# Optimization experiments

Measured on AMD Instinct MI355X. Metric: run time of the kernel, lower is better.

## Reference

```python
import jax, jax.numpy as jnp
import numpy as np

N = 100000   # nodes
E = 1600000  # edges
R = 8        # num_relations = 2 * n_speakers**2, n_speakers=2
G = 128      # g_dim
H1 = 64      # h1_dim
H2 = 64      # h2_dim (heads=1, concat)
NEG_SLOPE_ATT = 0.2   # RGATConv default negative_slope
NEG_SLOPE_OUT = 0.01  # F.leaky_relu default
BN_EPS = 1e-5


def setup_inputs() -> dict:
    key = jax.random.key(0)
    ks = jax.random.split(key, 13)
    node_features = jax.random.normal(ks[0], (N, G), dtype=jnp.float32)
    edge_index = jax.random.randint(ks[1], (2, E), 0, N, dtype=jnp.int64)
    edge_type = jax.random.randint(ks[2], (E,), 0, R, dtype=jnp.int64)
    # RGATConv layer 1: per-relation weight [R, in, heads*out], q/k [heads*out, heads], bias
    W1 = jax.random.normal(ks[3], (R, G, H1), dtype=jnp.float32) / np.float32(np.sqrt(G))
    q1 = jax.random.normal(ks[4], (H1, 1), dtype=jnp.float32) / np.float32(np.sqrt(H1))
    k1 = jax.random.normal(ks[5], (H1, 1), dtype=jnp.float32) / np.float32(np.sqrt(H1))
    b1 = jnp.zeros((H1,), dtype=jnp.float32)
    # RGATConv layer 2
    W2 = jax.random.normal(ks[6], (R, H1, H2), dtype=jnp.float32) / np.float32(np.sqrt(H1))
    q2 = jax.random.normal(ks[7], (H2, 1), dtype=jnp.float32) / np.float32(np.sqrt(H2))
    k2 = jax.random.normal(ks[8], (H2, 1), dtype=jnp.float32) / np.float32(np.sqrt(H2))
    b2 = jnp.zeros((H2,), dtype=jnp.float32)
    # BatchNorm1d affine params
    gamma = jnp.ones((H2,), dtype=jnp.float32)
    beta = jnp.zeros((H2,), dtype=jnp.float32)
    return {"node_features": node_features, "edge_index": edge_index,
            "edge_type": edge_type, "W1": W1, "q1": q1, "k1": k1, "b1": b1,
            "W2": W2, "q2": q2, "k2": k2, "b2": b2, "gamma": gamma, "beta": beta}


def _rgat_conv(x, src, dst, edge_type, W, q, k, b):
    # Per-relation dense transform for all nodes: [R, N, O] (R is small = 8)
    xw = jnp.einsum('ni,rio->rno', x, W)
    # Per-edge transformed endpoint features (gathered by relation + node id)
    hi = xw[edge_type, dst]   # [E, O] target-side
    hj = xw[edge_type, src]   # [E, O] source-side (message content)
    # Additive self-attention, across-relation softmax over incoming edges of dst
    alpha = jax.nn.leaky_relu(hi @ q + hj @ k, NEG_SLOPE_ATT)  # [E, 1]
    n = x.shape[0]
    m = jax.ops.segment_max(alpha, dst, num_segments=n)
    m = jnp.where(jnp.isfinite(m), m, 0.0)  # nodes with no in-edges
    e = jnp.exp(alpha - m[dst])
    denom = jax.ops.segment_sum(e, dst, num_segments=n)
    a = e / (denom[dst] + 1e-16)
    # Weighted scatter-add aggregation (heads=1, concat)
    out = jax.ops.segment_sum(hj * a, dst, num_segments=n)  # [N, O]
    return out + b


def reference(node_features, edge_index, edge_type, W1, q1, k1, b1,
              W2, q2, k2, b2, gamma, beta):
    src = edge_index[0]  # source j (messages flow src -> dst)
    dst = edge_index[1]  # target i
    x = _rgat_conv(node_features, src, dst, edge_type, W1, q1, k1, b1)
    x = jax.nn.relu(x)
    x = _rgat_conv(x, src, dst, edge_type, W2, q2, k2, b2)
    # BatchNorm1d (training-mode batch statistics, biased variance)
    mean = jnp.mean(x, axis=0)
    var = jnp.var(x, axis=0)
    x = (x - mean) * jax.lax.rsqrt(var + BN_EPS) * gamma + beta
    return jax.nn.leaky_relu(x, NEG_SLOPE_OUT)
```

## Files before the change

kernel.cpp:

```cpp
#include <hip/hip_runtime.h>
#include <hip/hip_bf16.h>

#define NN 100000
#define EE 1600000
#define RR 8
#define NBKT 391
#define ACHUNK 2048
#define CAP 5120
#define NB_NODES ((NN + 63) / 64)

typedef __attribute__((ext_vector_type(8))) short bf16x8;
typedef __attribute__((ext_vector_type(4))) float f32x4;

__device__ __forceinline__ unsigned short f2bf(float v) {
    __hip_bfloat16 h = __float2bfloat16(v);
    return *reinterpret_cast<unsigned short*>(&h);
}
__device__ __forceinline__ float bf2f(unsigned short u) {
    unsigned x = (unsigned)u << 16;
    return __uint_as_float(x);
}

template<int IN_DIM>
__device__ __forceinline__ void wt_frag_dev(const float* __restrict__ W,
                                            unsigned short* __restrict__ Wf,
                                            int r, int blk, int nb) {
    constexpr int KSTEPS = IN_DIM / 32;
    for (int i = blk * 256 + threadIdx.x; i < IN_DIM * 64; i += nb * 256) {
        int k = i >> 6, o = i & 63;
        int ks = k >> 5, quad = (k >> 3) & 3, j = k & 7;
        int tl = o >> 4, l16 = o & 15;
        int lane = quad * 16 + l16;
        size_t idx = ((((size_t)r * KSTEPS + ks) * 4 + tl) * 64 + lane) * 8 + j;
        Wf[idx] = f2bf(W[((size_t)r * IN_DIM + k) * 64 + o]);
    }
}

template<int IN_DIM>
__device__ __forceinline__ void wqk_frag_dev(const float* __restrict__ W,
        const float* __restrict__ q, const float* __restrict__ k,
        unsigned short* __restrict__ Sf, int blk, int nb) {
    for (int i = blk * 256 + threadIdx.x; i < IN_DIM * 16; i += nb * 256) {
        int j = i & 7, lane = (i >> 3) & 63, ks = i >> 9;
        int col = lane & 15, quad = lane >> 4;
        int kd = ks * 32 + quad * 8 + j;
        const float* v = (col < 8) ? q : k;
        int r = (col < 8) ? col : col - 8;
        float s = 0.f;
        #pragma unroll
        for (int o = 0; o < 64; o++) s += W[((size_t)r * IN_DIM + kd) * 64 + o] * v[o];
        Sf[i] = f2bf(s);
    }
}

__global__ __launch_bounds__(256)
void prep(const float* __restrict__ W1, const float* __restrict__ q1, const float* __restrict__ k1,
          const float* __restrict__ W2, const float* __restrict__ q2, const float* __restrict__ k2,
          unsigned short* __restrict__ Wf1, unsigned short* __restrict__ Wf2,
          unsigned short* __restrict__ Sf1, unsigned short* __restrict__ Sf2,
          unsigned* __restrict__ bcnt, float* __restrict__ stats)
{
    int b = blockIdx.x;
    if (b < 16)       wt_frag_dev<128>(W1, Wf1, b >> 1, b & 1, 2);
    else if (b < 32)  wt_frag_dev<64>(W2, Wf2, (b - 16) >> 1, b & 1, 2);
    else if (b < 48)  wqk_frag_dev<128>(W1, q1, k1, Sf1, b - 32, 16);
    else if (b < 52)  wqk_frag_dev<64>(W2, q2, k2, Sf2, b - 48, 4);
    else {
        int t = threadIdx.x;
        for (int i = t; i < NBKT; i += 256) bcnt[i] = 0;
        if (t < 128) stats[t] = 0.f;
    }
}

__global__ __launch_bounds__(256)
void part_scatter(const int* __restrict__ src, const int* __restrict__ dst,
                  const int* __restrict__ et, unsigned* __restrict__ bcnt,
                  unsigned* __restrict__ tmp) {
    __shared__ unsigned h[NBKT], base[NBKT];
    int t = threadIdx.x;
    for (int i = t; i < NBKT; i += 256) h[i] = 0;
    __syncthreads();
    int e0 = blockIdx.x * ACHUNK;
    for (int i = t; i < ACHUNK; i += 256) {
        int e = e0 + i;
        if (e < EE) atomicAdd(&h[((unsigned)dst[e]) >> 8], 1u);
    }
    __syncthreads();
    for (int i = t; i < NBKT; i += 256) {
        base[i] = (unsigned)i * CAP + (h[i] ? atomicAdd(&bcnt[i], h[i]) : 0u);
        h[i] = 0;
    }
    __syncthreads();
    for (int i = t; i < ACHUNK; i += 256) {
        int e = e0 + i;
        if (e < EE) {
            unsigned d = (unsigned)dst[e];
            unsigned bk = d >> 8;
            unsigned off = atomicAdd(&h[bk], 1u);
            unsigned pos = base[bk] + off;
            if (pos < (bk + 1u) * CAP) {
                unsigned val = ((d & 255u) << 23) | ((unsigned)et[e] << 20) | (unsigned)src[e];
                tmp[pos] = val;
            }
        }
    }
}

__global__ __launch_bounds__(256)
void bucket_csr(const unsigned* __restrict__ bcnt, const unsigned* __restrict__ tmp,
                unsigned* __restrict__ rowstart, unsigned* __restrict__ rowdeg,
                unsigned* __restrict__ pk) {
    __shared__ unsigned lcnt[256], lscan[256], lrs[256];
    int b = blockIdx.x, t = threadIdx.x;
    unsigned ebeg = (unsigned)b * CAP;
    unsigned cnt = min(bcnt[b], (unsigned)CAP);
    unsigned eend = ebeg + cnt;
    lcnt[t] = 0;
    __syncthreads();
    for (unsigned i = ebeg + t; i < eend; i += 256)
        atomicAdd(&lcnt[tmp[i] >> 23], 1u);
    __syncthreads();
    unsigned v = lcnt[t];
    lscan[t] = v;
    __syncthreads();
    for (int off = 1; off < 256; off <<= 1) {
        unsigned u = (t >= off) ? lscan[t - off] : 0u;
        __syncthreads();
        lscan[t] += u;
        __syncthreads();
    }
    unsigned excl = lscan[t] - v;
    lrs[t] = ebeg + excl;
    int node = b * 256 + t;
    if (node < NN) { rowstart[node] = ebeg + excl; rowdeg[node] = v; }
    lcnt[t] = 0;
    __syncthreads();
    for (unsigned i = ebeg + t; i < eend; i += 256) {
        unsigned val = tmp[i];
        unsigned d = val >> 23;
        unsigned pos = lrs[d] + atomicAdd(&lcnt[d], 1u);
        pk[pos] = val & 0x7FFFFFu;
    }
}

template<int IN_DIM, bool BF16IN>
__global__ __launch_bounds__(256)
void gemm_mfma(const void* __restrict__ xv, const unsigned short* __restrict__ Wf,
               const unsigned short* __restrict__ Sf,
               unsigned short* __restrict__ xw,
               float* __restrict__ sq, float* __restrict__ sk,
               float* __restrict__ gmax)
{
    constexpr int KSTEPS = IN_DIM / 32;
    constexpr int NB = IN_DIM / 8;
    constexpr int WITEMS = KSTEPS * 4 * 64;
    __shared__ alignas(16) unsigned short xl[64 * IN_DIM];
    __shared__ alignas(16) unsigned short wl[WITEMS * 8];
    __shared__ float smax[4][8];

    const int n0 = blockIdx.x * 64;
    const int t = threadIdx.x;
    const int wave = t >> 6, lane = t & 63;
    const int quad = lane >> 4, l16 = lane & 15;

    for (int c = t; c < 64 * IN_DIM / 4; c += 256) {
        int row = c / (IN_DIM / 4), kc = (c % (IN_DIM / 4)) * 4;
        int gr = n0 + row;
        ushort4 u = make_ushort4(0, 0, 0, 0);
        if constexpr (BF16IN) {
            if (gr < NN) u = *(const ushort4*)((const unsigned short*)xv + (size_t)gr * IN_DIM + kc);
        } else {
            if (gr < NN) {
                float4 v = *(const float4*)((const float*)xv + (size_t)gr * IN_DIM + kc);
                u.x = f2bf(v.x); u.y = f2bf(v.y); u.z = f2bf(v.z); u.w = f2bf(v.w);
            }
        }
        int b = kc >> 3;
        *(ushort4*)&xl[row * IN_DIM + ((b ^ (row & (NB - 1))) << 3) + (kc & 7)] = u;
    }
    __syncthreads();

    bf16x8 afr[KSTEPS];
    const int arow = wave * 16 + l16;
    #pragma unroll
    for (int ks = 0; ks < KSTEPS; ks++) {
        int b = ks * 4 + quad;
        afr[ks] = *(const bf16x8*)&xl[arow * IN_DIM + ((b ^ (arow & (NB - 1))) << 3)];
    }

    {
        f32x4 accs = {0.f, 0.f, 0.f, 0.f};
        #pragma unroll
        for (int ks = 0; ks < KSTEPS; ks++) {
            bf16x8 sfr = *(const bf16x8*)&Sf[(ks * 64 + lane) * 8];
            accs = __builtin_amdgcn_mfma_f32_16x16x32_bf16(afr[ks], sfr, accs, 0, 0, 0);
        }
        float pm = -1e30f;
        #pragma unroll
        for (int reg = 0; reg < 4; reg++) {
            int grow = n0 + wave * 16 + quad * 4 + reg;
            if (grow < NN) {
                if (l16 < 8) sq[(size_t)l16 * NN + grow] = accs[reg];
                else { sk[(size_t)(l16 - 8) * NN + grow] = accs[reg]; pm = fmaxf(pm, accs[reg]); }
            }
        }
        pm = fmaxf(pm, __shfl_xor(pm, 16, 64));
        pm = fmaxf(pm, __shfl_xor(pm, 32, 64));
        if (quad == 0 && l16 >= 8) smax[wave][l16 - 8] = pm;
    }
    __syncthreads();
    if (t < 8) {
        float v = fmaxf(fmaxf(smax[0][t], smax[1][t]), fmaxf(smax[2][t], smax[3][t]));
        gmax[blockIdx.x * 8 + t] = v;
    }

    #pragma unroll 1
    for (int r = 0; r < RR; r++) {
        const unsigned short* Wr = Wf + (size_t)r * WITEMS * 8;
        #pragma unroll
        for (int i = t; i < WITEMS; i += 256)
            *(bf16x8*)&wl[(size_t)i * 8] = *(const bf16x8*)(Wr + (size_t)i * 8);
        __syncthreads();

        bf16x8 bfr[KSTEPS][4];
        #pragma unroll
        for (int ks = 0; ks < KSTEPS; ks++)
            #pragma unroll
            for (int tl = 0; tl < 4; tl++)
                bfr[ks][tl] = *(const bf16x8*)&wl[(size_t)((ks * 4 + tl) * 64 + lane) * 8];

        f32x4 acc[4] = {{0.f,0.f,0.f,0.f},{0.f,0.f,0.f,0.f},{0.f,0.f,0.f,0.f},{0.f,0.f,0.f,0.f}};
        #pragma unroll
        for (int ks = 0; ks < KSTEPS; ks++)
            #pragma unroll
            for (int tl = 0; tl < 4; tl++)
                acc[tl] = __builtin_amdgcn_mfma_f32_16x16x32_bf16(afr[ks], bfr[ks][tl], acc[tl], 0, 0, 0);

        const size_t rbase = (size_t)r * NN;
        #pragma unroll
        for (int reg = 0; reg < 4; reg++) {
            int grow = n0 + wave * 16 + quad * 4 + reg;
            if (grow < NN) {
                ushort4 u;
                u.x = f2bf(acc[0][reg]); u.y = f2bf(acc[1][reg]);
                u.z = f2bf(acc[2][reg]); u.w = f2bf(acc[3][reg]);
                *(ushort4*)(xw + (rbase + grow) * 64 + l16 * 4) = u;
            }
        }
        __syncthreads();
    }
}

__global__ __launch_bounds__(256)
void max_reduce(const float* __restrict__ gmax, float* __restrict__ mxk) {
    __shared__ float smr[32][8];
    int t = threadIdx.x;
    int r = t & 7, grp = t >> 3;
    float m0 = -1e30f, m1 = -1e30f, m2 = -1e30f, m3 = -1e30f;
    for (int i = grp; i < NB_NODES; i += 128) {
        m0 = fmaxf(m0, gmax[i * 8 + r]);
        int i1 = i + 32, i2 = i + 64, i3 = i + 96;
        if (i1 < NB_NODES) m1 = fmaxf(m1, gmax[i1 * 8 + r]);
        if (i2 < NB_NODES) m2 = fmaxf(m2, gmax[i2 * 8 + r]);
        if (i3 < NB_NODES) m3 = fmaxf(m3, gmax[i3 * 8 + r]);
    }
    smr[grp][r] = fmaxf(fmaxf(m0, m1), fmaxf(m2, m3));
    __syncthreads();
    if (t < 8) {
        float mm = smr[0][t];
        #pragma unroll
        for (int g2 = 1; g2 < 32; g2++) mm = fmaxf(mm, smr[g2][t]);
        mxk[t] = mm;
    }
}

template<int LAYER>
__global__ __launch_bounds__(256)
void node_aggregate(const unsigned* __restrict__ rowstart, const unsigned* __restrict__ rowdeg,
                    const unsigned* __restrict__ pk,
                    const float* __restrict__ sq, const float* __restrict__ sk,
                    const float* __restrict__ mxk,
                    const unsigned short* __restrict__ xw, const float* __restrict__ b,
                    void* __restrict__ outv)
{
    const int node = blockIdx.x * 4 + (threadIdx.x >> 6);
    const int lane = threadIdx.x & 63;
    const int g = lane >> 4, c16 = lane & 15;
    const unsigned beg = rowstart[node];
    const unsigned deg = rowdeg[node];
    const unsigned end = beg + deg;

    const float sqreg = sq[(size_t)(lane & 7) * NN + node];
    float tmx = sqreg + mxk[lane & 7];
    tmx = fmaxf(tmx, __shfl_xor(tmx, 1, 64));
    tmx = fmaxf(tmx, __shfl_xor(tmx, 2, 64));
    tmx = fmaxf(tmx, __shfl_xor(tmx, 4, 64));
    const float m = tmx > 0.f ? tmx : 0.2f * tmx;

    float a0 = 0.f, a1 = 0.f, a2 = 0.f, a3 = 0.f, den = 0.f;
    for (unsigned c0 = beg; c0 < end; c0 += 64) {
        unsigned i = c0 + lane;
        unsigned p = 0;
        if (i < end) p = pk[i];
        unsigned r = p >> 20;
        unsigned rowidx = r * NN + (p & 0xFFFFFu);
        float skv = sk[rowidx];
        float sqv_e = __shfl(sqreg, (int)r, 64);
        float a = sqv_e + skv;
        a = a > 0.f ? a : 0.2f * a;
        float w = __expf(a - m);
        if (i >= end) w = 0.f;
        den += w;
        int cnt8 = ((int)min(64u, end - c0) + 7) & ~7;
        for (int j = 0; j < cnt8; j += 8) {
            float    w0 = __shfl(w, j + g, 64);
            unsigned r0 = (unsigned)__shfl((int)rowidx, j + g, 64);
            float    w1 = __shfl(w, j + 4 + g, 64);
            unsigned r1 = (unsigned)__shfl((int)rowidx, j + 4 + g, 64);
            ushort4 v0 = *(const ushort4*)(xw + (size_t)r0 * 64 + c16 * 4);
            ushort4 v1 = *(const ushort4*)(xw + (size_t)r1 * 64 + c16 * 4);
            a0 += w0 * bf2f(v0.x) + w1 * bf2f(v1.x);
            a1 += w0 * bf2f(v0.y) + w1 * bf2f(v1.y);
            a2 += w0 * bf2f(v0.z) + w1 * bf2f(v1.z);
            a3 += w0 * bf2f(v0.w) + w1 * bf2f(v1.w);
        }
    }
    #pragma unroll
    for (int off = 32; off >= 1; off >>= 1)
        den += __shfl_xor(den, off, 64);
    a0 += __shfl_xor(a0, 16, 64); a0 += __shfl_xor(a0, 32, 64);
    a1 += __shfl_xor(a1, 16, 64); a1 += __shfl_xor(a1, 32, 64);
    a2 += __shfl_xor(a2, 16, 64); a2 += __shfl_xor(a2, 32, 64);
    a3 += __shfl_xor(a3, 16, 64); a3 += __shfl_xor(a3, 32, 64);

    float accg = (g == 0) ? a0 : (g == 1) ? a1 : (g == 2) ? a2 : a3;
    float res = (deg > 0) ? accg / (den + 1e-16f) : 0.f;
    int c = g * 16 + c16;
    if constexpr (LAYER == 1) {
        res += b[c];
        res = res > 0.f ? res : 0.f;
        ((unsigned short*)outv)[(size_t)node * 64 + c] = f2bf(res);
    } else {
        ((float*)outv)[(size_t)node * 64 + c] = res;
    }
}

__global__ __launch_bounds__(256)
void bn_stats(const float* __restrict__ x, float* __restrict__ stats)
{
    int c = threadIdx.x & 63;
    int w = threadIdx.x >> 6;
    float s = 0.f, s2 = 0.f;
    for (int row = blockIdx.x * 4 + w; row < NN; row += gridDim.x * 4) {
        float v = x[(size_t)row * 64 + c];
        s += v; s2 += v * v;
    }
    __shared__ float ls[4][64], ls2[4][64];
    ls[w][c] = s; ls2[w][c] = s2;
    __syncthreads();
    if (threadIdx.x < 64) {
        atomicAdd(&stats[c],      ls[0][c] + ls[1][c] + ls[2][c] + ls[3][c]);
        atomicAdd(&stats[64 + c], ls2[0][c] + ls2[1][c] + ls2[2][c] + ls2[3][c]);
    }
}

__global__ __launch_bounds__(256)
void bn_apply(float* __restrict__ x, const float* __restrict__ stats,
              const float* __restrict__ gamma, const float* __restrict__ beta)
{
    int i = blockIdx.x * 256 + threadIdx.x;
    if (i >= NN * 64) return;
    int c = i & 63;
    float mean = stats[c] * (1.f / NN);
    float var  = stats[64 + c] * (1.f / NN) - mean * mean;
    float sc   = rsqrtf(var + 1e-5f) * gamma[c];
    float v = (x[i] - mean) * sc + beta[c];
    x[i] = v > 0.f ? v : 0.01f * v;
}

extern "C" void kernel_launch(void* const* d_in, const int* in_sizes, int n_in,
                              void* d_out, int out_size, void* d_ws, size_t ws_size,
                              hipStream_t stream)
{
    const float* x0 = (const float*)d_in[0];
    const int*   ei = (const int*)d_in[1];
    const int*   et = (const int*)d_in[2];
    const float* W1 = (const float*)d_in[3];
    const float* q1 = (const float*)d_in[4];
    const float* k1 = (const float*)d_in[5];
    const float* b1 = (const float*)d_in[6];
    const float* W2 = (const float*)d_in[7];
    const float* q2 = (const float*)d_in[8];
    const float* k2 = (const float*)d_in[9];
    const float* gamma = (const float*)d_in[11];
    const float* beta  = (const float*)d_in[12];
    const int* src = ei;
    const int* dst = ei + EE;
    float* out = (float*)d_out;

    char* base = (char*)d_ws;
    size_t off = 0;
    auto take = [&](size_t bytes) -> char* {
        char* p = base + off;
        off = (off + bytes + 255) & ~(size_t)255;
        return p;
    };
    float*    sq       = (float*)take((size_t)RR * NN * 4);
    float*    sk       = (float*)take((size_t)RR * NN * 4);
    unsigned* rowstart = (unsigned*)take((size_t)NN * 4);
    unsigned* rowdeg   = (unsigned*)take((size_t)NN * 4);
    unsigned* bcnt     = (unsigned*)take((size_t)NBKT * 4);
    unsigned* tmp      = (unsigned*)take((size_t)NBKT * CAP * 4);
    unsigned* pk       = (unsigned*)take((size_t)NBKT * CAP * 4);
    unsigned short* x1 = (unsigned short*)take((size_t)NN * 64 * 2);
    float*    stats    = (float*)take(512);
    float*    gmax     = (float*)take((size_t)NB_NODES * 8 * 4);
    float*    mxk1     = (float*)take(RR * 4);
    float*    mxk2     = (float*)take(RR * 4);
    unsigned short* Wf1 = (unsigned short*)take((size_t)RR * 128 * 64 * 2);
    unsigned short* Wf2 = (unsigned short*)take((size_t)RR * 64 * 64 * 2);
    unsigned short* Sf1 = (unsigned short*)take((size_t)128 * 16 * 2);
    unsigned short* Sf2 = (unsigned short*)take((size_t)64 * 16 * 2);
    unsigned short* xw  = (unsigned short*)take((size_t)RR * NN * 64 * 2);

    const int nb_part  = (EE + ACHUNK - 1) / ACHUNK;
    const int nb_agg   = NN / 4;
    const int nb_elem  = (NN * 64) / 256;

    prep<<<53, 256, 0, stream>>>(W1, q1, k1, W2, q2, k2, Wf1, Wf2, Sf1, Sf2,
                                 bcnt, stats);
    part_scatter<<<nb_part, 256, 0, stream>>>(src, dst, et, bcnt, tmp);
    bucket_csr<<<NBKT, 256, 0, stream>>>(bcnt, tmp, rowstart, rowdeg, pk);

    gemm_mfma<128, false><<<NB_NODES, 256, 0, stream>>>(x0, Wf1, Sf1, xw, sq, sk, gmax);
    max_reduce<<<1, 256, 0, stream>>>(gmax, mxk1);
    node_aggregate<1><<<nb_agg, 256, 0, stream>>>(rowstart, rowdeg, pk, sq, sk, mxk1,
                                                  xw, b1, x1);

    gemm_mfma<64, true><<<NB_NODES, 256, 0, stream>>>(x1, Wf2, Sf2, xw, sq, sk, gmax);
    max_reduce<<<1, 256, 0, stream>>>(gmax, mxk2);
    node_aggregate<2><<<nb_agg, 256, 0, stream>>>(rowstart, rowdeg, pk, sq, sk, mxk2,
                                                  xw, nullptr, out);

    bn_stats<<<512, 256, 0, stream>>>(out, stats);
    bn_apply<<<nb_elem, 256, 0, stream>>>(out, stats, gamma, beta);
}
```

Before: 414.5 us.

## Fuse edge partitioning into prep and CSR build into first GEMM launch

Merges the weight-prep kernel with the edge partition/scatter kernel, and runs the per-bucket CSR construction as extra blocks of the layer-1 GEMM launch, so independent work overlaps and two launches disappear. The bucket counter reset moves to a hipMemsetAsync, since the scatter blocks now run in the same launch as prep. This trades launch overhead and serialization for larger shared-memory footprints in the fused kernels, which could lower occupancy of the GEMM blocks.

```diff
diff --git a/kernel.cpp b/kernel.cpp
--- a/kernel.cpp
+++ b/kernel.cpp
@@ -8,6 +8,7 @@
 #define ACHUNK 2048
 #define CAP 5120
 #define NB_NODES ((NN + 63) / 64)
+#define NB_PART ((EE + ACHUNK - 1) / ACHUNK)
 
 typedef __attribute__((ext_vector_type(8))) short bf16x8;
 typedef __attribute__((ext_vector_type(4))) float f32x4;
@@ -54,64 +55,66 @@
 }
 
 __global__ __launch_bounds__(256)
-void prep(const float* __restrict__ W1, const float* __restrict__ q1, const float* __restrict__ k1,
-          const float* __restrict__ W2, const float* __restrict__ q2, const float* __restrict__ k2,
-          unsigned short* __restrict__ Wf1, unsigned short* __restrict__ Wf2,
-          unsigned short* __restrict__ Sf1, unsigned short* __restrict__ Sf2,
-          unsigned* __restrict__ bcnt, float* __restrict__ stats)
-{
-    int b = blockIdx.x;
+void prep_scatter(const float* __restrict__ W1, const float* __restrict__ q1,
+                  const float* __restrict__ k1,
+                  const float* __restrict__ W2, const float* __restrict__ q2,
+                  const float* __restrict__ k2,
+                  unsigned short* __restrict__ Wf1, unsigned short* __restrict__ Wf2,
+                  unsigned short* __restrict__ Sf1, unsigned short* __restrict__ Sf2,
+                  float* __restrict__ stats,
+                  const int* __restrict__ src, const int* __restrict__ dst,
+                  const int* __restrict__ et,
+                  unsigned* __restrict__ bcnt, unsigned* __restrict__ tmp)
+{
+    __shared__ unsigned h[NBKT], base[NBKT];
+    int bb = blockIdx.x;
+    if (bb < NB_PART) {
+        int t = threadIdx.x;
+        for (int i = t; i < NBKT; i += 256) h[i] = 0;
+        __syncthreads();
+        int e0 = bb * ACHUNK;
+        for (int i = t; i < ACHUNK; i += 256) {
+            int e = e0 + i;
+            if (e < EE) atomicAdd(&h[((unsigned)dst[e]) >> 8], 1u);
+        }
+        __syncthreads();
+        for (int i = t; i < NBKT; i += 256) {
+            base[i] = (unsigned)i * CAP + (h[i] ? atomicAdd(&bcnt[i], h[i]) : 0u);
+            h[i] = 0;
+        }
+        __syncthreads();
+        for (int i = t; i < ACHUNK; i += 256) {
+            int e = e0 + i;
+            if (e < EE) {
+                unsigned d = (unsigned)dst[e];
+                unsigned bk = d >> 8;
+                unsigned off = atomicAdd(&h[bk], 1u);
+                unsigned pos = base[bk] + off;
+                if (pos < (bk + 1u) * CAP) {
+                    unsigned val = ((d & 255u) << 23) | ((unsigned)et[e] << 20) | (unsigned)src[e];
+                    tmp[pos] = val;
+                }
+            }
+        }
+        return;
+    }
+    int b = bb - NB_PART;
     if (b < 16)       wt_frag_dev<128>(W1, Wf1, b >> 1, b & 1, 2);
     else if (b < 32)  wt_frag_dev<64>(W2, Wf2, (b - 16) >> 1, b & 1, 2);
     else if (b < 48)  wqk_frag_dev<128>(W1, q1, k1, Sf1, b - 32, 16);
     else if (b < 52)  wqk_frag_dev<64>(W2, q2, k2, Sf2, b - 48, 4);
     else {
         int t = threadIdx.x;
-        for (int i = t; i < NBKT; i += 256) bcnt[i] = 0;
         if (t < 128) stats[t] = 0.f;
     }
 }
 
-__global__ __launch_bounds__(256)
-void part_scatter(const int* __restrict__ src, const int* __restrict__ dst,
-                  const int* __restrict__ et, unsigned* __restrict__ bcnt,
-                  unsigned* __restrict__ tmp) {
-    __shared__ unsigned h[NBKT], base[NBKT];
+__device__ __forceinline__ void bucket_csr_body(const unsigned* __restrict__ bcnt,
+        const unsigned* __restrict__ tmp, unsigned* __restrict__ rowstart,
+        unsigned* __restrict__ rowdeg, unsigned* __restrict__ pk, int b)
+{
+    __shared__ unsigned lcnt[256], lscan[256], lrs[256];
     int t = threadIdx.x;
-    for (int i = t; i < NBKT; i += 256) h[i] = 0;
-    __syncthreads();
-    int e0 = blockIdx.x * ACHUNK;
-    for (int i = t; i < ACHUNK; i += 256) {
-        int e = e0 + i;
-        if (e < EE) atomicAdd(&h[((unsigned)dst[e]) >> 8], 1u);
-    }
-    __syncthreads();
-    for (int i = t; i < NBKT; i += 256) {
-        base[i] = (unsigned)i * CAP + (h[i] ? atomicAdd(&bcnt[i], h[i]) : 0u);
-        h[i] = 0;
-    }
-    __syncthreads();
-    for (int i = t; i < ACHUNK; i += 256) {
-        int e = e0 + i;
-        if (e < EE) {
-            unsigned d = (unsigned)dst[e];
-            unsigned bk = d >> 8;
-            unsigned off = atomicAdd(&h[bk], 1u);
-            unsigned pos = base[bk] + off;
-            if (pos < (bk + 1u) * CAP) {
-                unsigned val = ((d & 255u) << 23) | ((unsigned)et[e] << 20) | (unsigned)src[e];
-                tmp[pos] = val;
-            }
-        }
-    }
-}
-
-__global__ __launch_bounds__(256)
-void bucket_csr(const unsigned* __restrict__ bcnt, const unsigned* __restrict__ tmp,
-                unsigned* __restrict__ rowstart, unsigned* __restrict__ rowdeg,
-                unsigned* __restrict__ pk) {
-    __shared__ unsigned lcnt[256], lscan[256], lrs[256];
-    int b = blockIdx.x, t = threadIdx.x;
     unsigned ebeg = (unsigned)b * CAP;
     unsigned cnt = min(bcnt[b], (unsigned)CAP);
     unsigned eend = ebeg + cnt;
@@ -145,11 +148,14 @@
 
 template<int IN_DIM, bool BF16IN>
 __global__ __launch_bounds__(256)
-void gemm_mfma(const void* __restrict__ xv, const unsigned short* __restrict__ Wf,
-               const unsigned short* __restrict__ Sf,
-               unsigned short* __restrict__ xw,
-               float* __restrict__ sq, float* __restrict__ sk,
-               float* __restrict__ gmax)
+void gemm_csr(const void* __restrict__ xv, const unsigned short* __restrict__ Wf,
+              const unsigned short* __restrict__ Sf,
+              unsigned short* __restrict__ xw,
+              float* __restrict__ sq, float* __restrict__ sk,
+              float* __restrict__ gmax,
+              const unsigned* __restrict__ bcnt, const unsigned* __restrict__ tmp,
+              unsigned* __restrict__ rowstart, unsigned* __restrict__ rowdeg,
+              unsigned* __restrict__ pk, int with_csr)
 {
     constexpr int KSTEPS = IN_DIM / 32;
     constexpr int NB = IN_DIM / 8;
@@ -158,7 +164,13 @@
     __shared__ alignas(16) unsigned short wl[WITEMS * 8];
     __shared__ float smax[4][8];
 
-    const int n0 = blockIdx.x * 64;
+    if (with_csr && blockIdx.x < NBKT) {
+        bucket_csr_body(bcnt, tmp, rowstart, rowdeg, pk, blockIdx.x);
+        return;
+    }
+    const int nblk = blockIdx.x - (with_csr ? NBKT : 0);
+
+    const int n0 = nblk * 64;
     const int t = threadIdx.x;
     const int wave = t >> 6, lane = t & 63;
     const int quad = lane >> 4, l16 = lane & 15;
@@ -211,7 +223,7 @@
     __syncthreads();
     if (t < 8) {
         float v = fmaxf(fmaxf(smax[0][t], smax[1][t]), fmaxf(smax[2][t], smax[3][t]));
-        gmax[blockIdx.x * 8 + t] = v;
+        gmax[nblk * 8 + t] = v;
     }
 
     #pragma unroll 1
@@ -423,21 +435,22 @@
     unsigned short* Sf2 = (unsigned short*)take((size_t)64 * 16 * 2);
     unsigned short* xw  = (unsigned short*)take((size_t)RR * NN * 64 * 2);
 
-    const int nb_part  = (EE + ACHUNK - 1) / ACHUNK;
     const int nb_agg   = NN / 4;
     const int nb_elem  = (NN * 64) / 256;
 
-    prep<<<53, 256, 0, stream>>>(W1, q1, k1, W2, q2, k2, Wf1, Wf2, Sf1, Sf2,
-                                 bcnt, stats);
-    part_scatter<<<nb_part, 256, 0, stream>>>(src, dst, et, bcnt, tmp);
-    bucket_csr<<<NBKT, 256, 0, stream>>>(bcnt, tmp, rowstart, rowdeg, pk);
-
-    gemm_mfma<128, false><<<NB_NODES, 256, 0, stream>>>(x0, Wf1, Sf1, xw, sq, sk, gmax);
+    hipMemsetAsync(bcnt, 0, (size_t)NBKT * 4, stream);
+    prep_scatter<<<NB_PART + 53, 256, 0, stream>>>(W1, q1, k1, W2, q2, k2,
+                                                   Wf1, Wf2, Sf1, Sf2, stats,
+                                                   src, dst, et, bcnt, tmp);
+
+    gemm_csr<128, false><<<NBKT + NB_NODES, 256, 0, stream>>>(
+        x0, Wf1, Sf1, xw, sq, sk, gmax, bcnt, tmp, rowstart, rowdeg, pk, 1);
     max_reduce<<<1, 256, 0, stream>>>(gmax, mxk1);
     node_aggregate<1><<<nb_agg, 256, 0, stream>>>(rowstart, rowdeg, pk, sq, sk, mxk1,
                                                   xw, b1, x1);
 
-    gemm_mfma<64, true><<<NB_NODES, 256, 0, stream>>>(x1, Wf2, Sf2, xw, sq, sk, gmax);
+    gemm_csr<64, true><<<NB_NODES, 256, 0, stream>>>(
+        x1, Wf2, Sf2, xw, sq, sk, gmax, bcnt, tmp, rowstart, rowdeg, pk, 0);
     max_reduce<<<1, 256, 0, stream>>>(gmax, mxk2);
     node_aggregate<2><<<nb_agg, 256, 0, stream>>>(rowstart, rowdeg, pk, sq, sk, mxk2,
                                                   xw, nullptr, out);
```

Result: faster. 397.8 us (-4.0%).
